# Performance work log

Hardware: AMD Instinct MI355X
Metric: run time of the kernel (lower is better)

Reference implementation:

```python
import jax, jax.numpy as jnp
import numpy as np

# SLAYER neuron / simulation hyperparameters (from network.yaml)
THETA = 10.0      # spike threshold
TAU_SR = 10.0     # SRM (PSP) kernel time constant [ms]
TAU_REF = 1.0     # refractory kernel time constant [ms]
SCALE_REF = 2.0   # refractory kernel scale
TS = 1.0          # simulation step [ms]
K_SRM = 100       # truncation length of SRM kernel (eps decays ~0 by 10*tau)
K_REF = 32        # truncation length of refractory kernel (tauRef=1 -> decays fast)


def _eps_kernel(tau, k):
    # eps(t) = (t/tau) * exp(1 - t/tau), eps(0) = 0  (SLAYER SRM alpha kernel)
    t = jnp.arange(k, dtype=jnp.float32) * TS
    return (t / tau) * jnp.exp(1.0 - t / tau)


def psp(x, kern):
    # Causal temporal filter: y[..., t] = sum_j kern[j] * x[..., t - j]
    B, N, T = x.shape
    lhs = x.reshape(B * N, 1, T)
    rhs = kern[::-1].reshape(1, 1, -1)  # lax.conv is cross-correlation -> flip
    y = jax.lax.conv_general_dilated(
        lhs, rhs, window_strides=(1,), padding=[(kern.shape[0] - 1, 0)],
        dimension_numbers=('NCH', 'OIH', 'NCH'))
    return y.reshape(B, N, T)


def spike(u, refk):
    # Sequential thresholding with refractory feedback (SLAYER spikeFunction fwd).
    # u: [B, N, T] membrane drive. State r: future refractory contributions.
    kr = refk.shape[0]
    refk_shift = jnp.concatenate([refk[1:], jnp.zeros((1,), refk.dtype)])

    def step(r, u_t):
        m = u_t + r[..., 0]                      # membrane potential at t
        s = (m >= THETA).astype(u_t.dtype)       # hard spike
        r_next = jnp.concatenate([r[..., 1:], jnp.zeros_like(r[..., :1])], -1) \
                 + s[..., None] * refk_shift     # add refractory response
        return r_next, s

    uT = jnp.moveaxis(u, -1, 0)                  # [T, B, N]
    r0 = jnp.zeros(uT.shape[1:] + (kr,), u.dtype)
    _, sT = jax.lax.scan(step, r0, uT)
    return jnp.moveaxis(sT, 0, -1) / TS          # [B, N, T]


def setup_inputs() -> dict:
    key = jax.random.key(0)
    k1, k2, k3 = jax.random.split(key, 3)
    B, NIN, NHID, NOUT, T = 32, 2048, 512, 10, 350
    spike_input = (jax.random.uniform(k1, (B, NIN, T)) < 0.05).astype(jnp.float32)
    W1 = jax.random.normal(k2, (NHID, NIN), dtype=jnp.float32) * 0.05
    W2 = jax.random.normal(k3, (NOUT, NHID), dtype=jnp.float32) * 0.05
    return {"spike_input": spike_input, "W1": W1, "W2": W2}


def reference(spike_input, W1, W2):
    srm = _eps_kernel(TAU_SR, K_SRM)
    refk = -SCALE_REF * THETA * _eps_kernel(TAU_REF, K_REF)
    # layer 1: psp -> dense -> spike
    a1 = jnp.einsum('bnt,mn->bmt', psp(spike_input, srm), W1)
    s1 = spike(a1, refk)
    # layer 2: psp -> dense -> spike
    a2 = jnp.einsum('bnt,mn->bmt', psp(s1, srm), W2)
    s2 = spike(a2, refk)
    return s2
```

## Files before the change

kernel.cpp:

```cpp
#include <hip/hip_runtime.h>
#include <stdint.h>

static constexpr int B  = 32;
static constexpr int T  = 350;
static constexpr int NIN = 2048;
static constexpr int NH  = 512;
static constexpr int NO  = 10;
static constexpr int BT  = B * T;

static constexpr float THETA = 10.0f;
static constexpr float BETA  = 0.36787944117144233f;
static constexpr float CREF  = 54.365636569180904707f;

static constexpr size_t OFF_W1T  = 0;
static constexpr size_t OFF_MASK = 4196352;
static constexpr size_t OFF_SRM  = 7080960;
static constexpr size_t OFF_Z1   = 7081984;
static constexpr size_t OFF_A1   = 30019584;
static constexpr size_t OFF_LST  = OFF_A1;
static constexpr size_t OFF_CNT  = OFF_A1 + 4300800;
static constexpr size_t OFF_Z2   = OFF_Z1;

__global__ void __launch_bounds__(256) k_prep(const float* __restrict__ x,
                                              const float* __restrict__ W1,
                                              float* __restrict__ W1T,
                                              uint64_t* __restrict__ mask,
                                              float* __restrict__ srm28) {
    int bid = blockIdx.x;
    if (bid < 1024) {
        __shared__ uint64_t tb[6][64];
        int b = bid >> 5, nblk = bid & 31;
        int wv = threadIdx.x >> 6, lane = threadIdx.x & 63;
        for (int g = 0; g < 4; ++g) {
            float v[4][6];
            #pragma unroll
            for (int i = 0; i < 4; ++i) {
                int nr = wv + 4 * (4 * g + i);
                const float* xp = x + ((size_t)b * NIN + nblk * 64 + nr) * T;
                #pragma unroll
                for (int c = 0; c < 6; ++c) {
                    int t = c * 64 + lane;
                    v[i][c] = (t < T) ? xp[t] : 0.f;
                }
            }
            #pragma unroll
            for (int i = 0; i < 4; ++i) {
                int nr = wv + 4 * (4 * g + i);
                #pragma unroll
                for (int c = 0; c < 6; ++c) {
                    uint64_t mk = __ballot(v[i][c] != 0.0f);
                    if (lane == 0) tb[c][nr] = mk;
                }
            }
        }
        __syncthreads();
        static const uint64_t AM[6] = {
            0x00000000FFFFFFFFull, 0x0000FFFF0000FFFFull, 0x00FF00FF00FF00FFull,
            0x0F0F0F0F0F0F0F0Full, 0x3333333333333333ull, 0x5555555555555555ull };
        for (int c = wv; c < 6; c += 4) {
            uint64_t w = tb[c][lane];
            #pragma unroll
            for (int i = 0; i < 6; ++i) {
                int s = 32 >> i;
                uint64_t A = AM[i];
                uint64_t y = __shfl_xor((unsigned long long)w, s);
                if ((lane & s) == 0) w = (w & A)  | ((y & A) << s);
                else                 w = (w & ~A) | ((y & ~A) >> s);
            }
            int t = c * 64 + lane;
            if (t < T) mask[((size_t)b * 32 + nblk) * 352 + t] = w;
        }
    } else if (bid < 2048) {
        __shared__ float tile[32][33];
        int idx = bid - 1024;
        int n0 = (idx & 63) * 32, m0 = (idx >> 6) * 32;
        int tx = threadIdx.x & 31, ty0 = threadIdx.x >> 5;
        #pragma unroll
        for (int i = 0; i < 4; ++i) {
            int ty = ty0 + 8 * i;
            tile[ty][tx] = W1[(size_t)(m0 + ty) * NIN + n0 + tx];
        }
        __syncthreads();
        #pragma unroll
        for (int i = 0; i < 4; ++i) {
            int ty = ty0 + 8 * i;
            W1T[(size_t)(n0 + ty) * NH + m0 + tx] = tile[tx][ty];
        }
    } else {
        int j = threadIdx.x;
        if (j < 192) {
            float v = 0.f;
            int i = j - 28;
            if (i >= 0 && i < 100) { float t = (float)i; v = (t * 0.1f) * expf(1.f - t * 0.1f); }
            srm28[j] = v;
        }
        for (int i = j; i < NH; i += 256) W1T[(size_t)2048 * NH + i] = 0.f;
    }
}

__global__ void __launch_bounds__(64) k_decode(const uint64_t* __restrict__ mask,
                                               uint16_t* __restrict__ glst,
                                               int* __restrict__ gcnt) {
    __shared__ uint16_t lst[192];
    int t = blockIdx.x, b = blockIdx.y;
    int row = b * T + t;
    int lane = threadIdx.x;
    uint64_t w = (lane < 32) ? mask[((size_t)b * 32 + lane) * 352 + t] : 0ull;
    int cnt = __popcll(w);
    int pre = cnt;
    #pragma unroll
    for (int off = 1; off < 64; off <<= 1) {
        int v = __shfl_up(pre, off);
        if (lane >= off) pre += v;
    }
    int total = __shfl(pre, 63);
    int excl = pre - cnt;
    while (w) {
        int bit = __builtin_ctzll(w);
        w &= w - 1;
        lst[excl++] = (uint16_t)((lane << 6) + bit);
    }
    int padded = (total + 7) & ~7;
    if (lane < padded - total) lst[total + lane] = 2048;
    __syncthreads();
    uint16_t* op = glst + (size_t)row * 192;
    for (int i = lane; i < padded; i += 64) op[i] = lst[i];
    if (lane == 0) gcnt[row] = padded;
}

template<int H>
__global__ void __launch_bounds__(64) k_z1g(const uint16_t* __restrict__ glst,
                                            const int* __restrict__ gcnt,
                                            const float* __restrict__ W1T,
                                            float* __restrict__ z1) {
    int row = blockIdx.x, lane = threadIdx.x;
    int padded = gcnt[row];
    const ushort4* lp = (const ushort4*)(glst + (size_t)row * 192);
    const float4* W4 = (const float4*)W1T;
    float4 acc = {0, 0, 0, 0};
    int idx = H * 64 + lane;
    for (int k = 0; k < padded; k += 8) {
        ushort4 q0 = lp[k >> 2];
        ushort4 q1 = lp[(k >> 2) + 1];
        float4 x0 = W4[(size_t)q0.x * 128 + idx];
        float4 x1 = W4[(size_t)q0.y * 128 + idx];
        float4 x2 = W4[(size_t)q0.z * 128 + idx];
        float4 x3 = W4[(size_t)q0.w * 128 + idx];
        float4 x4 = W4[(size_t)q1.x * 128 + idx];
        float4 x5 = W4[(size_t)q1.y * 128 + idx];
        float4 x6 = W4[(size_t)q1.z * 128 + idx];
        float4 x7 = W4[(size_t)q1.w * 128 + idx];
        acc.x += x0.x; acc.y += x0.y; acc.z += x0.z; acc.w += x0.w;
        acc.x += x1.x; acc.y += x1.y; acc.z += x1.z; acc.w += x1.w;
        acc.x += x2.x; acc.y += x2.y; acc.z += x2.z; acc.w += x2.w;
        acc.x += x3.x; acc.y += x3.y; acc.z += x3.z; acc.w += x3.w;
        acc.x += x4.x; acc.y += x4.y; acc.z += x4.z; acc.w += x4.w;
        acc.x += x5.x; acc.y += x5.y; acc.z += x5.z; acc.w += x5.w;
        acc.x += x6.x; acc.y += x6.y; acc.z += x6.z; acc.w += x6.w;
        acc.x += x7.x; acc.y += x7.y; acc.z += x7.z; acc.w += x7.w;
    }
    ((float4*)(z1 + (size_t)row * NH))[idx] = acc;
}

__global__ void __launch_bounds__(64) k_fir1(const float* __restrict__ src,
                                             float* __restrict__ dst,
                                             const float* __restrict__ srm28) {
    __shared__ float tb[192];
    int b = blockIdx.x, half = blockIdx.y, tg = blockIdx.z;
    int lane = threadIdx.x;
    for (int i = lane; i < 192; i += 64) tb[i] = srm28[i];
    __syncthreads();
    int t0 = tg * 16;
    int m = half * 256 + lane * 4;
    const float* sp = src + (size_t)b * T * NH + m;

    float4 acc[16];
    #pragma unroll
    for (int r = 0; r < 16; ++r) acc[r] = make_float4(0.f, 0.f, 0.f, 0.f);
    float c[16];
    #pragma unroll
    for (int r = 0; r < 16; ++r) c[r] = tb[r + 127];

    for (int o = 0; o < 8; ++o) {
        #pragma unroll
        for (int j = 0; j < 16; ++j) {
            int dd = o * 16 + j;
            int tau = t0 - 99 + dd;
            float4 v = make_float4(0.f, 0.f, 0.f, 0.f);
            if (tau >= 0 && tau < T) v = *(const float4*)(sp + (size_t)tau * NH);
            #pragma unroll
            for (int r = 0; r < 16; ++r) {
                acc[r].x += c[r] * v.x; acc[r].y += c[r] * v.y;
                acc[r].z += c[r] * v.z; acc[r].w += c[r] * v.w;
            }
            #pragma unroll
            for (int r = 15; r > 0; --r) c[r] = c[r - 1];
            int ci = 126 - dd;
            c[0] = tb[ci < 0 ? 0 : ci];
        }
    }
    #pragma unroll
    for (int r = 0; r < 16; ++r) {
        int t = t0 + r;
        if (t < T) *(float4*)(dst + ((size_t)b * T + t) * NH + m) = acc[r];
    }
}

__global__ void __launch_bounds__(512) k_scanz2(const float* __restrict__ a1,
                                                const float* __restrict__ W2,
                                                float* __restrict__ z2) {
    __shared__ float w2s[NO * NH];
    __shared__ uint64_t smask[16][8];
    constexpr int CT = 16;
    constexpr int NC = (T + CT - 1) / CT;
    int b = blockIdx.x, tid = threadIdx.x;
    int wv = tid >> 6;
    for (int i = tid; i < NO * NH; i += 512) w2s[i] = W2[i];
    const float* up = a1 + (size_t)b * T * NH + tid;
    float A = 0.f, Bs = 0.f;
    float cur[CT], nxt[CT];
    #pragma unroll
    for (int j = 0; j < CT; ++j) cur[j] = up[(size_t)j * NH];
    __syncthreads();
    for (int c = 0; c < NC; ++c) {
        int t0 = c * CT;
        int nsteps = (T - t0 < CT) ? (T - t0) : CT;
        if (c + 1 < NC) {
            #pragma unroll
            for (int j = 0; j < CT; ++j) {
                int t = t0 + CT + j;
                nxt[j] = (t < T) ? up[(size_t)t * NH] : 0.f;
            }
        }
        #pragma unroll
        for (int j = 0; j < CT; ++j) {
            if (j < nsteps) {
                float mem = cur[j] - CREF * Bs;
                float sp = (mem >= THETA) ? 1.0f : 0.0f;
                A = sp + BETA * A;
                Bs = BETA * (Bs + A);
                uint64_t mk = __ballot(sp != 0.0f);
                if ((tid & 63) == 0) smask[j][wv] = mk;
            }
        }
        __syncthreads();
        if (tid < nsteps * NO) {
            int j = tid / NO, o = tid - j * NO;
            const float* wrow = w2s + o * NH;
            float acc = 0.f;
            #pragma unroll
            for (int w8 = 0; w8 < 8; ++w8) {
                uint64_t mk = smask[j][w8];
                int base = w8 * 64;
                while (mk) {
                    int bit = __builtin_ctzll(mk);
                    mk &= mk - 1;
                    acc += wrow[base + bit];
                }
            }
            z2[((size_t)b * T + t0 + j) * NO + o] = acc;
        }
        __syncthreads();
        #pragma unroll
        for (int j = 0; j < CT; ++j) cur[j] = nxt[j];
    }
}

__global__ void __launch_bounds__(256) k_fir2scan(const float* __restrict__ z2,
                                                  const float* __restrict__ srm28,
                                                  float* __restrict__ out) {
    __shared__ float tb[192];
    __shared__ float zb[350 * 11 + 16];
    __shared__ float ab[352 * 10];
    int b = blockIdx.x, tid = threadIdx.x;
    if (tid < 192) tb[tid] = srm28[tid];
    const float* zp = z2 + (size_t)b * T * NO;
    for (int i = tid; i < T * NO; i += 256) {
        int t = i / NO, o = i - t * NO;
        zb[t * 11 + o] = zp[i];
    }
    __syncthreads();
    if (tid < 220) {
        int tt = tid / 10, o = tid - tt * 10;
        int t0 = tt * 16;
        float acc[16];
        #pragma unroll
        for (int r = 0; r < 16; ++r) acc[r] = 0.f;
        float c[16];
        #pragma unroll
        for (int r = 0; r < 16; ++r) c[r] = tb[r + 127];
        for (int oo = 0; oo < 8; ++oo) {
            #pragma unroll
            for (int j = 0; j < 16; ++j) {
                int dd = oo * 16 + j;
                int tau = t0 - 99 + dd;
                float v = (tau >= 0 && tau < T) ? zb[tau * 11 + o] : 0.f;
                #pragma unroll
                for (int r = 0; r < 16; ++r) acc[r] += c[r] * v;
                #pragma unroll
                for (int r = 15; r > 0; --r) c[r] = c[r - 1];
                int ci = 126 - dd;
                c[0] = tb[ci < 0 ? 0 : ci];
            }
        }
        #pragma unroll
        for (int r = 0; r < 16; ++r) {
            int t = t0 + r;
            if (t < T) ab[t * 10 + o] = acc[r];
        }
    }
    __syncthreads();
    if (tid < NO) {
        int o = tid;
        float A = 0.f, Bs = 0.f;
        float* op = out + ((size_t)b * NO + o) * T;
        for (int t = 0; t < T; ++t) {
            float mem = ab[t * 10 + o] - CREF * Bs;
            float sp = (mem >= THETA) ? 1.0f : 0.0f;
            A = sp + BETA * A;
            Bs = BETA * (Bs + A);
            op[t] = sp;
        }
    }
}

extern "C" void kernel_launch(void* const* d_in, const int* in_sizes, int n_in,
                              void* d_out, int out_size, void* d_ws, size_t ws_size,
                              hipStream_t stream) {
    const float* x  = (const float*)d_in[0];
    const float* W1 = (const float*)d_in[1];
    const float* W2 = (const float*)d_in[2];
    char* ws = (char*)d_ws;
    float*    W1T  = (float*)(ws + OFF_W1T);
    uint64_t* mask = (uint64_t*)(ws + OFF_MASK);
    float*    srm  = (float*)(ws + OFF_SRM);
    float*    z1   = (float*)(ws + OFF_Z1);
    float*    a1   = (float*)(ws + OFF_A1);
    uint16_t* glst = (uint16_t*)(ws + OFF_LST);
    int*      gcnt = (int*)(ws + OFF_CNT);
    float*    z2   = (float*)(ws + OFF_Z2);
    float*    out  = (float*)d_out;

    hipLaunchKernelGGL(k_prep,       dim3(2049),     dim3(256), 0, stream, x, W1, W1T, mask, srm);
    hipLaunchKernelGGL(k_decode,     dim3(T, B),     dim3(64),  0, stream, mask, glst, gcnt);
    hipLaunchKernelGGL((k_z1g<0>),   dim3(BT),       dim3(64),  0, stream, glst, gcnt, W1T, z1);
    hipLaunchKernelGGL((k_z1g<1>),   dim3(BT),       dim3(64),  0, stream, glst, gcnt, W1T, z1);
    hipLaunchKernelGGL(k_fir1,       dim3(B, 2, 22), dim3(64),  0, stream, z1, a1, srm);
    hipLaunchKernelGGL(k_scanz2,     dim3(B),        dim3(512), 0, stream, a1, W2, z2);
    hipLaunchKernelGGL(k_fir2scan,   dim3(B),        dim3(256), 0, stream, z2, srm, out);
}
```

Measured before the change: 327.7 us.

## Stage sliced W1 columns in LDS and gather spikes from shared memory

Re-lays out the transposed W1 into 64 slices of 8 output features, each slice holding all 2049 input rows. A new kernel loads one slice (about 64KB) into LDS and then, for a chunk of time rows, sums the W1 rows selected by each row's spike list using LDS float4 reads. This replaces the two global-memory gather kernels. Global reads of W1 are amortized across many rows, but each block re-reads the spike lists for its rows, only 512 blocks run, and the large LDS footprint limits occupancy.

```diff
diff --git a/kernel.cpp b/kernel.cpp
--- a/kernel.cpp
+++ b/kernel.cpp
@@ -12,7 +12,7 @@
 static constexpr float BETA  = 0.36787944117144233f;
 static constexpr float CREF  = 54.365636569180904707f;
 
-static constexpr size_t OFF_W1T  = 0;
+static constexpr size_t OFF_W1TS = 0;
 static constexpr size_t OFF_MASK = 4196352;
 static constexpr size_t OFF_SRM  = 7080960;
 static constexpr size_t OFF_Z1   = 7081984;
@@ -21,9 +21,13 @@
 static constexpr size_t OFF_CNT  = OFF_A1 + 4300800;
 static constexpr size_t OFF_Z2   = OFF_Z1;
 
+static constexpr int SLICE_F = 8;
+static constexpr int NSLICE  = NH / SLICE_F;
+static constexpr int SLICE_STRIDE = 2049 * SLICE_F;
+
 __global__ void __launch_bounds__(256) k_prep(const float* __restrict__ x,
                                               const float* __restrict__ W1,
-                                              float* __restrict__ W1T,
+                                              float* __restrict__ W1Ts,
                                               uint64_t* __restrict__ mask,
                                               float* __restrict__ srm28) {
     int bid = blockIdx.x;
@@ -84,7 +88,8 @@
         #pragma unroll
         for (int i = 0; i < 4; ++i) {
             int ty = ty0 + 8 * i;
-            W1T[(size_t)(n0 + ty) * NH + m0 + tx] = tile[tx][ty];
+            int n = n0 + ty, m = m0 + tx;
+            W1Ts[(size_t)(m >> 3) * SLICE_STRIDE + n * SLICE_F + (m & 7)] = tile[tx][ty];
         }
     } else {
         int j = threadIdx.x;
@@ -94,7 +99,8 @@
             if (i >= 0 && i < 100) { float t = (float)i; v = (t * 0.1f) * expf(1.f - t * 0.1f); }
             srm28[j] = v;
         }
-        for (int i = j; i < NH; i += 256) W1T[(size_t)2048 * NH + i] = 0.f;
+        for (int i = j; i < NSLICE * SLICE_F; i += 256)
+            W1Ts[(size_t)(i >> 3) * SLICE_STRIDE + 2048 * SLICE_F + (i & 7)] = 0.f;
     }
 }
 
@@ -128,38 +134,48 @@
     if (lane == 0) gcnt[row] = padded;
 }
 
-template<int H>
-__global__ void __launch_bounds__(64) k_z1g(const uint16_t* __restrict__ glst,
-                                            const int* __restrict__ gcnt,
-                                            const float* __restrict__ W1T,
-                                            float* __restrict__ z1) {
-    int row = blockIdx.x, lane = threadIdx.x;
-    int padded = gcnt[row];
-    const ushort4* lp = (const ushort4*)(glst + (size_t)row * 192);
-    const float4* W4 = (const float4*)W1T;
-    float4 acc = {0, 0, 0, 0};
-    int idx = H * 64 + lane;
-    for (int k = 0; k < padded; k += 8) {
-        ushort4 q0 = lp[k >> 2];
-        ushort4 q1 = lp[(k >> 2) + 1];
-        float4 x0 = W4[(size_t)q0.x * 128 + idx];
-        float4 x1 = W4[(size_t)q0.y * 128 + idx];
-        float4 x2 = W4[(size_t)q0.z * 128 + idx];
-        float4 x3 = W4[(size_t)q0.w * 128 + idx];
-        float4 x4 = W4[(size_t)q1.x * 128 + idx];
-        float4 x5 = W4[(size_t)q1.y * 128 + idx];
-        float4 x6 = W4[(size_t)q1.z * 128 + idx];
-        float4 x7 = W4[(size_t)q1.w * 128 + idx];
-        acc.x += x0.x; acc.y += x0.y; acc.z += x0.z; acc.w += x0.w;
-        acc.x += x1.x; acc.y += x1.y; acc.z += x1.z; acc.w += x1.w;
-        acc.x += x2.x; acc.y += x2.y; acc.z += x2.z; acc.w += x2.w;
-        acc.x += x3.x; acc.y += x3.y; acc.z += x3.z; acc.w += x3.w;
-        acc.x += x4.x; acc.y += x4.y; acc.z += x4.z; acc.w += x4.w;
-        acc.x += x5.x; acc.y += x5.y; acc.z += x5.z; acc.w += x5.w;
-        acc.x += x6.x; acc.y += x6.y; acc.z += x6.z; acc.w += x6.w;
-        acc.x += x7.x; acc.y += x7.y; acc.z += x7.z; acc.w += x7.w;
-    }
-    ((float4*)(z1 + (size_t)row * NH))[idx] = acc;
+__global__ void __launch_bounds__(256) k_z1s(const uint16_t* __restrict__ glst,
+                                             const int* __restrict__ gcnt,
+                                             const float* __restrict__ W1Ts,
+                                             float* __restrict__ z1) {
+    __shared__ float w1s[SLICE_STRIDE];
+    int s = blockIdx.x;
+    int bt0 = blockIdx.y * (BT / 8);
+    const float4* src = (const float4*)(W1Ts + (size_t)s * SLICE_STRIDE);
+    for (int i = threadIdx.x; i < SLICE_STRIDE / 4; i += 256)
+        ((float4*)w1s)[i] = src[i];
+    __syncthreads();
+
+    int q  = threadIdx.x & 1;
+    int rl = threadIdx.x >> 1;
+    for (int rr = rl; rr < BT / 8; rr += 128) {
+        int row = bt0 + rr;
+        int padded = gcnt[row];
+        const ushort4* lp = (const ushort4*)(glst + (size_t)row * 192);
+        float4 acc = {0, 0, 0, 0};
+        for (int k = 0; k < padded; k += 8) {
+            ushort4 q0 = lp[k >> 2];
+            ushort4 q1 = lp[(k >> 2) + 1];
+            const float* base = w1s + q * 4;
+            float4 x0 = *(const float4*)(base + q0.x * SLICE_F);
+            float4 x1 = *(const float4*)(base + q0.y * SLICE_F);
+            float4 x2 = *(const float4*)(base + q0.z * SLICE_F);
+            float4 x3 = *(const float4*)(base + q0.w * SLICE_F);
+            float4 x4 = *(const float4*)(base + q1.x * SLICE_F);
+            float4 x5 = *(const float4*)(base + q1.y * SLICE_F);
+            float4 x6 = *(const float4*)(base + q1.z * SLICE_F);
+            float4 x7 = *(const float4*)(base + q1.w * SLICE_F);
+            acc.x += x0.x; acc.y += x0.y; acc.z += x0.z; acc.w += x0.w;
+            acc.x += x1.x; acc.y += x1.y; acc.z += x1.z; acc.w += x1.w;
+            acc.x += x2.x; acc.y += x2.y; acc.z += x2.z; acc.w += x2.w;
+            acc.x += x3.x; acc.y += x3.y; acc.z += x3.z; acc.w += x3.w;
+            acc.x += x4.x; acc.y += x4.y; acc.z += x4.z; acc.w += x4.w;
+            acc.x += x5.x; acc.y += x5.y; acc.z += x5.z; acc.w += x5.w;
+            acc.x += x6.x; acc.y += x6.y; acc.z += x6.z; acc.w += x6.w;
+            acc.x += x7.x; acc.y += x7.y; acc.z += x7.z; acc.w += x7.w;
+        }
+        *(float4*)(z1 + (size_t)row * NH + s * SLICE_F + q * 4) = acc;
+    }
 }
 
 __global__ void __launch_bounds__(64) k_fir1(const float* __restrict__ src,
@@ -331,7 +347,7 @@
     const float* W1 = (const float*)d_in[1];
     const float* W2 = (const float*)d_in[2];
     char* ws = (char*)d_ws;
-    float*    W1T  = (float*)(ws + OFF_W1T);
+    float*    W1Ts = (float*)(ws + OFF_W1TS);
     uint64_t* mask = (uint64_t*)(ws + OFF_MASK);
     float*    srm  = (float*)(ws + OFF_SRM);
     float*    z1   = (float*)(ws + OFF_Z1);
@@ -341,11 +357,10 @@
     float*    z2   = (float*)(ws + OFF_Z2);
     float*    out  = (float*)d_out;
 
-    hipLaunchKernelGGL(k_prep,       dim3(2049),     dim3(256), 0, stream, x, W1, W1T, mask, srm);
-    hipLaunchKernelGGL(k_decode,     dim3(T, B),     dim3(64),  0, stream, mask, glst, gcnt);
-    hipLaunchKernelGGL((k_z1g<0>),   dim3(BT),       dim3(64),  0, stream, glst, gcnt, W1T, z1);
-    hipLaunchKernelGGL((k_z1g<1>),   dim3(BT),       dim3(64),  0, stream, glst, gcnt, W1T, z1);
-    hipLaunchKernelGGL(k_fir1,       dim3(B, 2, 22), dim3(64),  0, stream, z1, a1, srm);
-    hipLaunchKernelGGL(k_scanz2,     dim3(B),        dim3(512), 0, stream, a1, W2, z2);
-    hipLaunchKernelGGL(k_fir2scan,   dim3(B),        dim3(256), 0, stream, z2, srm, out);
-}
+    hipLaunchKernelGGL(k_prep,       dim3(2049),      dim3(256), 0, stream, x, W1, W1Ts, mask, srm);
+    hipLaunchKernelGGL(k_decode,     dim3(T, B),      dim3(64),  0, stream, mask, glst, gcnt);
+    hipLaunchKernelGGL(k_z1s,        dim3(NSLICE, 8), dim3(256), 0, stream, glst, gcnt, W1Ts, z1);
+    hipLaunchKernelGGL(k_fir1,       dim3(B, 2, 22),  dim3(64),  0, stream, z1, a1, srm);
+    hipLaunchKernelGGL(k_scanz2,     dim3(B),         dim3(512), 0, stream, a1, W2, z2);
+    hipLaunchKernelGGL(k_fir2scan,   dim3(B),         dim3(256), 0, stream, z2, srm, out);
+}
```

After: 310.5 us. 5.3% less time.

## Stage W1 column slices in LDS for sparse spike-gather matmul

Applied to the files above, without the earlier changes.

Replaces the two global-memory gather kernels for layer-1 dense accumulation with one kernel. Each block loads a 32-column by 512-input slice of W1 into shared memory and accumulates 352 rows, one input quarter at a time. W1 is re-laid out in quarter-blocked tiles, and the decode kernel now records per-quarter prefix counts instead of padded totals, which removes the sentinel zero row. This trades scattered global/L2 gathers for LDS reads with reuse across rows. The cost is a 64KB LDS footprint that limits occupancy, repeated reads of the spike lists per column slice, and only 512 blocks.

```diff
diff --git a/kernel.cpp b/kernel.cpp
--- a/kernel.cpp
+++ b/kernel.cpp
@@ -12,18 +12,18 @@
 static constexpr float BETA  = 0.36787944117144233f;
 static constexpr float CREF  = 54.365636569180904707f;
 
-static constexpr size_t OFF_W1T  = 0;
-static constexpr size_t OFF_MASK = 4196352;
-static constexpr size_t OFF_SRM  = 7080960;
-static constexpr size_t OFF_Z1   = 7081984;
-static constexpr size_t OFF_A1   = 30019584;
+static constexpr size_t OFF_W1TQ = 0;
+static constexpr size_t OFF_MASK = 4194304;
+static constexpr size_t OFF_SRM  = 7077888;
+static constexpr size_t OFF_Z1   = 7078912;
+static constexpr size_t OFF_A1   = 30016512;
 static constexpr size_t OFF_LST  = OFF_A1;
 static constexpr size_t OFF_CNT  = OFF_A1 + 4300800;
 static constexpr size_t OFF_Z2   = OFF_Z1;
 
 __global__ void __launch_bounds__(256) k_prep(const float* __restrict__ x,
                                               const float* __restrict__ W1,
-                                              float* __restrict__ W1T,
+                                              float* __restrict__ W1TQ,
                                               uint64_t* __restrict__ mask,
                                               float* __restrict__ srm28) {
     int bid = blockIdx.x;
@@ -81,10 +81,12 @@
             tile[ty][tx] = W1[(size_t)(m0 + ty) * NIN + n0 + tx];
         }
         __syncthreads();
+        int s = m0 >> 5, q = n0 >> 9;
+        size_t base = ((size_t)(s * 4 + q) * 512 + (n0 & 511)) * 32;
         #pragma unroll
         for (int i = 0; i < 4; ++i) {
             int ty = ty0 + 8 * i;
-            W1T[(size_t)(n0 + ty) * NH + m0 + tx] = tile[tx][ty];
+            W1TQ[base + (size_t)ty * 32 + tx] = tile[tx][ty];
         }
     } else {
         int j = threadIdx.x;
@@ -94,13 +96,12 @@
             if (i >= 0 && i < 100) { float t = (float)i; v = (t * 0.1f) * expf(1.f - t * 0.1f); }
             srm28[j] = v;
         }
-        for (int i = j; i < NH; i += 256) W1T[(size_t)2048 * NH + i] = 0.f;
     }
 }
 
 __global__ void __launch_bounds__(64) k_decode(const uint64_t* __restrict__ mask,
                                                uint16_t* __restrict__ glst,
-                                               int* __restrict__ gcnt) {
+                                               ushort4* __restrict__ gcnt) {
     __shared__ uint16_t lst[192];
     int t = blockIdx.x, b = blockIdx.y;
     int row = b * T + t;
@@ -113,53 +114,81 @@
         int v = __shfl_up(pre, off);
         if (lane >= off) pre += v;
     }
-    int total = __shfl(pre, 63);
+    int P0 = __shfl(pre, 7), P1 = __shfl(pre, 15), P2 = __shfl(pre, 23), P3 = __shfl(pre, 31);
     int excl = pre - cnt;
     while (w) {
         int bit = __builtin_ctzll(w);
         w &= w - 1;
         lst[excl++] = (uint16_t)((lane << 6) + bit);
     }
-    int padded = (total + 7) & ~7;
-    if (lane < padded - total) lst[total + lane] = 2048;
     __syncthreads();
     uint16_t* op = glst + (size_t)row * 192;
-    for (int i = lane; i < padded; i += 64) op[i] = lst[i];
-    if (lane == 0) gcnt[row] = padded;
-}
-
-template<int H>
-__global__ void __launch_bounds__(64) k_z1g(const uint16_t* __restrict__ glst,
-                                            const int* __restrict__ gcnt,
-                                            const float* __restrict__ W1T,
-                                            float* __restrict__ z1) {
-    int row = blockIdx.x, lane = threadIdx.x;
-    int padded = gcnt[row];
-    const ushort4* lp = (const ushort4*)(glst + (size_t)row * 192);
-    const float4* W4 = (const float4*)W1T;
-    float4 acc = {0, 0, 0, 0};
-    int idx = H * 64 + lane;
-    for (int k = 0; k < padded; k += 8) {
-        ushort4 q0 = lp[k >> 2];
-        ushort4 q1 = lp[(k >> 2) + 1];
-        float4 x0 = W4[(size_t)q0.x * 128 + idx];
-        float4 x1 = W4[(size_t)q0.y * 128 + idx];
-        float4 x2 = W4[(size_t)q0.z * 128 + idx];
-        float4 x3 = W4[(size_t)q0.w * 128 + idx];
-        float4 x4 = W4[(size_t)q1.x * 128 + idx];
-        float4 x5 = W4[(size_t)q1.y * 128 + idx];
-        float4 x6 = W4[(size_t)q1.z * 128 + idx];
-        float4 x7 = W4[(size_t)q1.w * 128 + idx];
-        acc.x += x0.x; acc.y += x0.y; acc.z += x0.z; acc.w += x0.w;
-        acc.x += x1.x; acc.y += x1.y; acc.z += x1.z; acc.w += x1.w;
-        acc.x += x2.x; acc.y += x2.y; acc.z += x2.z; acc.w += x2.w;
-        acc.x += x3.x; acc.y += x3.y; acc.z += x3.z; acc.w += x3.w;
-        acc.x += x4.x; acc.y += x4.y; acc.z += x4.z; acc.w += x4.w;
-        acc.x += x5.x; acc.y += x5.y; acc.z += x5.z; acc.w += x5.w;
-        acc.x += x6.x; acc.y += x6.y; acc.z += x6.z; acc.w += x6.w;
-        acc.x += x7.x; acc.y += x7.y; acc.z += x7.z; acc.w += x7.w;
-    }
-    ((float4*)(z1 + (size_t)row * NH))[idx] = acc;
+    for (int i = lane; i < P3; i += 64) op[i] = lst[i];
+    if (lane == 0) gcnt[row] = make_ushort4((uint16_t)P0, (uint16_t)P1,
+                                            (uint16_t)P2, (uint16_t)P3);
+}
+
+__global__ void __launch_bounds__(256) k_z1f(const uint16_t* __restrict__ glst,
+                                             const ushort4* __restrict__ gcnt,
+                                             const float* __restrict__ W1TQ,
+                                             float* __restrict__ z1) {
+    __shared__ float w1s[512 * 32];
+    int s = blockIdx.x;
+    int chunk = blockIdx.y;
+    int row0 = chunk * 352;
+    int tid = threadIdx.x;
+    int g = tid >> 3;
+    int e = tid & 7;
+
+    float4 acc[11];
+    #pragma unroll
+    for (int i = 0; i < 11; ++i) acc[i] = make_float4(0.f, 0.f, 0.f, 0.f);
+
+    for (int q = 0; q < 4; ++q) {
+        __syncthreads();
+        const float4* src = (const float4*)(W1TQ + ((size_t)s * 4 + q) * (512 * 32));
+        for (int i = tid; i < 512 * 8; i += 256) ((float4*)w1s)[i] = src[i];
+        __syncthreads();
+        #pragma unroll
+        for (int i = 0; i < 11; ++i) {
+            int row = row0 + g + 32 * i;
+            if (row >= BT) continue;
+            ushort4 C = gcnt[row];
+            int lo = (q == 0) ? 0 : (q == 1 ? C.x : (q == 2 ? C.y : C.z));
+            int hi = (q == 0) ? C.x : (q == 1 ? C.y : (q == 2 ? C.z : C.w));
+            const uint16_t* lp = glst + (size_t)row * 192;
+            const float* wb = w1s + e * 4;
+            float4 a = acc[i];
+            int k = lo;
+            if ((k & 1) && k < hi) {
+                int n = (int)lp[k] - (q << 9);
+                const float4 w0 = *(const float4*)(wb + (n << 5));
+                a.x += w0.x; a.y += w0.y; a.z += w0.z; a.w += w0.w;
+                ++k;
+            }
+            for (; k + 2 <= hi; k += 2) {
+                uint32_t pr = *(const uint32_t*)(lp + k);
+                int n0 = (int)(pr & 0xFFFFu) - (q << 9);
+                int n1 = (int)(pr >> 16) - (q << 9);
+                float4 w0 = *(const float4*)(wb + (n0 << 5));
+                float4 w1v = *(const float4*)(wb + (n1 << 5));
+                a.x += w0.x; a.y += w0.y; a.z += w0.z; a.w += w0.w;
+                a.x += w1v.x; a.y += w1v.y; a.z += w1v.z; a.w += w1v.w;
+            }
+            if (k < hi) {
+                int n = (int)lp[k] - (q << 9);
+                const float4 w0 = *(const float4*)(wb + (n << 5));
+                a.x += w0.x; a.y += w0.y; a.z += w0.z; a.w += w0.w;
+            }
+            acc[i] = a;
+        }
+    }
+    #pragma unroll
+    for (int i = 0; i < 11; ++i) {
+        int row = row0 + g + 32 * i;
+        if (row < BT)
+            *(float4*)(z1 + (size_t)row * NH + s * 32 + e * 4) = acc[i];
+    }
 }
 
 __global__ void __launch_bounds__(64) k_fir1(const float* __restrict__ src,
@@ -331,20 +360,19 @@
     const float* W1 = (const float*)d_in[1];
     const float* W2 = (const float*)d_in[2];
     char* ws = (char*)d_ws;
-    float*    W1T  = (float*)(ws + OFF_W1T);
+    float*    W1TQ = (float*)(ws + OFF_W1TQ);
     uint64_t* mask = (uint64_t*)(ws + OFF_MASK);
     float*    srm  = (float*)(ws + OFF_SRM);
     float*    z1   = (float*)(ws + OFF_Z1);
     float*    a1   = (float*)(ws + OFF_A1);
     uint16_t* glst = (uint16_t*)(ws + OFF_LST);
-    int*      gcnt = (int*)(ws + OFF_CNT);
+    ushort4*  gcnt = (ushort4*)(ws + OFF_CNT);
     float*    z2   = (float*)(ws + OFF_Z2);
     float*    out  = (float*)d_out;
 
-    hipLaunchKernelGGL(k_prep,       dim3(2049),     dim3(256), 0, stream, x, W1, W1T, mask, srm);
+    hipLaunchKernelGGL(k_prep,       dim3(2049),     dim3(256), 0, stream, x, W1, W1TQ, mask, srm);
     hipLaunchKernelGGL(k_decode,     dim3(T, B),     dim3(64),  0, stream, mask, glst, gcnt);
-    hipLaunchKernelGGL((k_z1g<0>),   dim3(BT),       dim3(64),  0, stream, glst, gcnt, W1T, z1);
-    hipLaunchKernelGGL((k_z1g<1>),   dim3(BT),       dim3(64),  0, stream, glst, gcnt, W1T, z1);
+    hipLaunchKernelGGL(k_z1f,        dim3(16, 32),   dim3(256), 0, stream, glst, gcnt, W1TQ, z1);
     hipLaunchKernelGGL(k_fir1,       dim3(B, 2, 22), dim3(64),  0, stream, z1, a1, srm);
     hipLaunchKernelGGL(k_scanz2,     dim3(B),        dim3(512), 0, stream, a1, W2, z2);
     hipLaunchKernelGGL(k_fir2scan,   dim3(B),        dim3(256), 0, stream, z2, srm, out);
```

Result: slower. 409.6 us (+25.0%).
